# Kernel optimization log

Measured on AMD Instinct MI355X. Metric: run time of the kernel, lower is better.

## Reference

```python
import jax, jax.numpy as jnp
import numpy as np

NUM_HEADS = 16


def setup_inputs() -> dict:
    key = jax.random.key(0)
    ks = jax.random.split(key, 6)
    B, S, D = 2, 2048, 1024
    hidden_states = jax.random.normal(ks[0], (B, S, D), dtype=jnp.float32)
    attention_mask = jnp.zeros((B, 1, 1, S), dtype=jnp.float32)  # additive mask
    # Linear weights stored as [in, out] (equivalent to torch weight.T)
    W_qkv = jax.random.normal(ks[1], (D, 3 * D), dtype=jnp.float32) * (1.0 / np.sqrt(D))
    b_qkv = jnp.zeros((3 * D,), dtype=jnp.float32)
    W_proj = jax.random.normal(ks[2], (D, D), dtype=jnp.float32) * (1.0 / np.sqrt(D))
    b_proj = jnp.zeros((D,), dtype=jnp.float32)
    return {
        "hidden_states": hidden_states,
        "attention_mask": attention_mask,
        "W_qkv": W_qkv,
        "b_qkv": b_qkv,
        "W_proj": W_proj,
        "b_proj": b_proj,
    }


def reference(hidden_states, attention_mask, W_qkv, b_qkv, W_proj, b_proj):
    B, S, D = hidden_states.shape
    H = NUM_HEADS
    hd = D // H
    scale = 1.0 / jnp.sqrt(jnp.asarray(hd, hidden_states.dtype))

    qkv = hidden_states @ W_qkv + b_qkv            # [B,S,3D]
    q, k, v = jnp.split(qkv, 3, axis=-1)
    # [B,S,D] -> [B,H,S,hd]
    split_heads = lambda t: t.reshape(B, S, H, hd).transpose(0, 2, 1, 3)
    q, k, v = split_heads(q), split_heads(k), split_heads(v)

    scores = jnp.einsum("bhqd,bhkd->bhqk", q, k) * scale + attention_mask
    attn = jax.nn.softmax(scores, axis=-1)
    ctx = jnp.einsum("bhqk,bhkd->bhqd", attn, v)   # [B,H,S,hd]
    ctx = ctx.transpose(0, 2, 1, 3).reshape(B, S, D)
    return ctx @ W_proj + b_proj
```

## Files before the change

### kernel.cpp

```cpp
#include <hip/hip_runtime.h>
#include <hip/hip_bf16.h>

typedef short short8 __attribute__((ext_vector_type(8)));
typedef float floatx4 __attribute__((ext_vector_type(4)));
typedef int intx4 __attribute__((ext_vector_type(4)));

#define S_LEN 2048
#define DMODEL 1024
#define NH 16
#define HD 64
#define BATCH 2

static __device__ __forceinline__ short f2bf(float x) {
    __hip_bfloat16 h = __float2bfloat16(x);
    return *(short*)&h;
}

static __device__ __forceinline__ unsigned pk2(float lo, float hi) {
    unsigned a = (unsigned)(unsigned short)f2bf(lo);
    unsigned b = (unsigned)(unsigned short)f2bf(hi);
    return a | (b << 16);
}

static __device__ __forceinline__ void async_ld16(const __hip_bfloat16* g, __hip_bfloat16* l) {
    __builtin_amdgcn_global_load_lds(
        (const __attribute__((address_space(1))) unsigned int*)g,
        (__attribute__((address_space(3))) unsigned int*)l, 16, 0, 0);
}

__global__ __launch_bounds__(256) void cvt_kernel(const float* __restrict__ X,
                                                  __hip_bfloat16* __restrict__ Y) {
    int i = (blockIdx.x * 256 + threadIdx.x) * 8;
    floatx4 f0 = *(const floatx4*)&X[i];
    floatx4 f1 = *(const floatx4*)&X[i + 4];
    short8 s;
    s[0] = f2bf(f0[0]); s[1] = f2bf(f0[1]); s[2] = f2bf(f0[2]); s[3] = f2bf(f0[3]);
    s[4] = f2bf(f1[0]); s[5] = f2bf(f1[1]); s[6] = f2bf(f1[2]); s[7] = f2bf(f1[3]);
    *(short8*)&Y[i] = s;
}

__global__ void transpose_kernel(const float* __restrict__ W,
                                 __hip_bfloat16* __restrict__ Wt, int K, int N) {
    __shared__ float tile[32][33];
    int n0 = blockIdx.x * 32, k0 = blockIdx.y * 32;
    int tx = threadIdx.x, ty = threadIdx.y;
#pragma unroll
    for (int i = 0; i < 32; i += 8)
        tile[ty + i][tx] = W[(size_t)(k0 + ty + i) * N + n0 + tx];
    __syncthreads();
#pragma unroll
    for (int i = 0; i < 32; i += 8)
        Wt[(size_t)(n0 + ty + i) * K + k0 + tx] = __float2bfloat16(tile[tx][ty + i]);
}

__global__ __launch_bounds__(256) void gemm128(
    const __hip_bfloat16* __restrict__ A, const __hip_bfloat16* __restrict__ Bt,
    const float* __restrict__ bias, float* __restrict__ Cf,
    __hip_bfloat16* __restrict__ Qp, __hip_bfloat16* __restrict__ Kp,
    __hip_bfloat16* __restrict__ Vt, int M, int N, int K, int mode) {
    __shared__ __align__(16) __hip_bfloat16 As[128 * 32];
    __shared__ __align__(16) __hip_bfloat16 Bs[128 * 32];
    const int m0 = blockIdx.y * 128, n0 = blockIdx.x * 128;
    const int t = threadIdx.x;
    const int wave = t >> 6, lane = t & 63;
    const int quad = lane >> 4, m16 = lane & 15;
    const int wm = (wave >> 1) * 64, wn = (wave & 1) * 64;
    const int srow = lane >> 2, scol = (lane & 3) * 8;

    floatx4 acc[4][4] = {};
    for (int k0 = 0; k0 < K; k0 += 32) {
#pragma unroll
        for (int i = 0; i < 2; i++) {
            const int rbase = wave * 32 + i * 16;
            async_ld16(&A[(size_t)(m0 + rbase + srow) * K + k0 + scol], &As[rbase * 32]);
            async_ld16(&Bt[(size_t)(n0 + rbase + srow) * K + k0 + scol], &Bs[rbase * 32]);
        }
        __syncthreads();
        short8 af[4], bfr[4];
#pragma unroll
        for (int i = 0; i < 4; i++)
            af[i] = *(const short8*)&As[(wm + i * 16 + m16) * 32 + quad * 8];
#pragma unroll
        for (int j = 0; j < 4; j++)
            bfr[j] = *(const short8*)&Bs[(wn + j * 16 + m16) * 32 + quad * 8];
#pragma unroll
        for (int i = 0; i < 4; i++)
#pragma unroll
            for (int j = 0; j < 4; j++)
                acc[i][j] = __builtin_amdgcn_mfma_f32_16x16x32_bf16(af[i], bfr[j], acc[i][j], 0, 0, 0);
        __syncthreads();
    }
#pragma unroll
    for (int i = 0; i < 4; i++)
#pragma unroll
        for (int j = 0; j < 4; j++) {
            int col = n0 + wn + j * 16 + m16;
            float bv = bias[col];
#pragma unroll
            for (int r = 0; r < 4; r++) {
                int row = m0 + wm + i * 16 + quad * 4 + r;
                float v = acc[i][j][r] + bv;
                if (mode == 0) {
                    Cf[(size_t)row * N + col] = v;
                } else {
                    __hip_bfloat16 hv = __float2bfloat16(v);
                    int tt = col >> 10, rem = col & 1023;
                    int h = rem >> 6, d = rem & 63;
                    int b = row >> 11, s = row & 2047;
                    if (tt == 0)      Qp[((size_t)(b * NH + h) * S_LEN + s) * HD + d] = hv;
                    else if (tt == 1) Kp[((size_t)(b * NH + h) * S_LEN + s) * HD + d] = hv;
                    else              Vt[((size_t)(b * NH + h) * HD + d) * S_LEN + s] = hv;
                }
            }
        }
}

__global__ __launch_bounds__(512, 8) void attn_kernel(
    const __hip_bfloat16* __restrict__ Q,
    const __hip_bfloat16* __restrict__ K,
    const __hip_bfloat16* __restrict__ Vt,
    const float* __restrict__ mask,
    __hip_bfloat16* __restrict__ ctx) {
    __shared__ __align__(16) __hip_bfloat16 smem[16384];
    const int bh = blockIdx.x;
    const int b = bh >> 4, h = bh & 15;
    const int t = threadIdx.x, wave = t >> 6, lane = t & 63;
    const int team = wave >> 2, tw = wave & 3;
    const int quad = lane >> 4, m16 = lane & 15;
    const int qbase = blockIdx.y * 64 + tw * 16;
    const int ko = team * (S_LEN / 2);
    const __hip_bfloat16* Qh = Q + (size_t)bh * S_LEN * HD;
    const __hip_bfloat16* Kh = K + (size_t)bh * S_LEN * HD;
    const __hip_bfloat16* Vh = Vt + (size_t)bh * HD * S_LEN;
    const float* mb = mask + (size_t)b * S_LEN;
    const float LOG2E = 1.44269504f;
    const float scale2 = 0.125f * LOG2E;
    const float M_FIX2 = 20.0f * LOG2E;

    __hip_bfloat16* Ksb = smem + team * 8192;
    __hip_bfloat16* Vsb = smem + team * 8192 + 4096;

    const int kr = lane >> 3, kc = lane & 7;
    const int kgoff = (tw * 8 + kr) * HD + ((kc ^ kr) * 8);
    const int vr = lane >> 2, vc = lane & 3;
    const int vd = tw * 16 + vr;
    const int vgoff = vd * S_LEN + (((vc ^ ((vd >> 1) & 3))) * 8);
    __hip_bfloat16* kdst0 = Ksb + tw * 512;
    __hip_bfloat16* kdst1 = Ksb + 2048 + tw * 512;
    __hip_bfloat16* vdst0 = Vsb + tw * 512;
    __hip_bfloat16* vdst1 = Vsb + 2048 + tw * 512;

    short8 aq0 = *(const short8*)&Qh[(size_t)(qbase + m16) * HD + quad * 8];
    short8 aq1 = *(const short8*)&Qh[(size_t)(qbase + m16) * HD + 32 + quad * 8];

    const short ONEB = (short)0x3F80;
    const short8 ones = {ONEB, ONEB, ONEB, ONEB, ONEB, ONEB, ONEB, ONEB};

    async_ld16(&Kh[(size_t)ko * HD + kgoff], kdst0);
    async_ld16(&Vh[(size_t)ko + vgoff], vdst0);
    __syncthreads();

    floatx4 o[4] = {};
    floatx4 lacc = {};
    const int swk = m16 & 7;
    const int e = quad & 1;
    const int C = ((quad & 1) << 1) | (quad >> 1);
    const int vsl = (C ^ ((m16 >> 1) & 3)) * 8;

    const int NIT = (S_LEN / 2) / 32;
    for (int it = 0; it < NIT; it++) {
        const int k0 = it * 32;
        const int cur = it & 1;
        if (it < NIT - 1) {
            async_ld16(&Kh[(size_t)(ko + k0 + 32) * HD + kgoff], cur ? kdst0 : kdst1);
            async_ld16(&Vh[(size_t)(ko + k0 + 32) + vgoff], cur ? vdst0 : vdst1);
        }

        const __hip_bfloat16* Kc = Ksb + cur * 2048;
        floatx4 sc[2] = {};
        __builtin_amdgcn_s_setprio(1);
#pragma unroll
        for (int kt = 0; kt < 2; kt++) {
            const int row = kt * 16 + m16;
            short8 ak0 = *(const short8*)&Kc[row * 64 + ((quad ^ swk) * 8)];
            short8 ak1 = *(const short8*)&Kc[row * 64 + (((quad + 4) ^ swk) * 8)];
            sc[kt] = __builtin_amdgcn_mfma_f32_16x16x32_bf16(ak0, aq0, sc[kt], 0, 0, 0);
            sc[kt] = __builtin_amdgcn_mfma_f32_16x16x32_bf16(ak1, aq1, sc[kt], 0, 0, 0);
        }
        __builtin_amdgcn_s_setprio(0);

        unsigned dk[2][2];
#pragma unroll
        for (int kt = 0; kt < 2; kt++) {
            floatx4 mv = *(const floatx4*)&mb[ko + k0 + kt * 16 + quad * 4];
            float p0 = __builtin_amdgcn_exp2f(
                __builtin_fmaf(sc[kt][0], scale2, __builtin_fmaf(mv[0], LOG2E, -M_FIX2)));
            float p1 = __builtin_amdgcn_exp2f(
                __builtin_fmaf(sc[kt][1], scale2, __builtin_fmaf(mv[1], LOG2E, -M_FIX2)));
            float p2 = __builtin_amdgcn_exp2f(
                __builtin_fmaf(sc[kt][2], scale2, __builtin_fmaf(mv[2], LOG2E, -M_FIX2)));
            float p3 = __builtin_amdgcn_exp2f(
                __builtin_fmaf(sc[kt][3], scale2, __builtin_fmaf(mv[3], LOG2E, -M_FIX2)));
            dk[kt][0] = pk2(p0, p1);
            dk[kt][1] = pk2(p2, p3);
        }

        unsigned s0 = e ? dk[0][0] : dk[1][0];
        unsigned s1 = e ? dk[0][1] : dk[1][1];
        unsigned r0 = (unsigned)__builtin_amdgcn_ds_swizzle((int)s0, 0x401F);
        unsigned r1 = (unsigned)__builtin_amdgcn_ds_swizzle((int)s1, 0x401F);
        intx4 wa;
        wa[0] = (int)(e ? r0 : dk[0][0]);
        wa[1] = (int)(e ? r1 : dk[0][1]);
        wa[2] = (int)(e ? dk[1][0] : r0);
        wa[3] = (int)(e ? dk[1][1] : r1);
        short8 ap = *(short8*)&wa;

        const __hip_bfloat16* Vc = Vsb + cur * 2048;
        __builtin_amdgcn_s_setprio(1);
        lacc = __builtin_amdgcn_mfma_f32_16x16x32_bf16(ap, ones, lacc, 0, 0, 0);
#pragma unroll
        for (int tt = 0; tt < 4; tt++) {
            const int d = tt * 16 + m16;
            short8 bv = *(const short8*)&Vc[d * 32 + vsl];
            o[tt] = __builtin_amdgcn_mfma_f32_16x16x32_bf16(ap, bv, o[tt], 0, 0, 0);
        }
        __builtin_amdgcn_s_setprio(0);
        __syncthreads();
    }

    float* xch = (float*)smem;
    const int xi = (tw * 64 + lane) * 21;
    if (team == 1) {
#pragma unroll
        for (int tt = 0; tt < 4; tt++)
#pragma unroll
            for (int r = 0; r < 4; r++) xch[xi + tt * 4 + r] = o[tt][r];
#pragma unroll
        for (int r = 0; r < 4; r++) xch[xi + 16 + r] = lacc[r];
    }
    __syncthreads();
    if (team == 0) {
        float li[4];
#pragma unroll
        for (int r = 0; r < 4; r++) li[r] = 1.0f / (lacc[r] + xch[xi + 16 + r]);
#pragma unroll
        for (int tt = 0; tt < 4; tt++)
#pragma unroll
            for (int r = 0; r < 4; r++) {
                int srow = qbase + quad * 4 + r;
                int d = tt * 16 + m16;
                float v = (o[tt][r] + xch[xi + tt * 4 + r]) * li[r];
                ctx[((size_t)b * S_LEN + srow) * DMODEL + h * HD + d] = __float2bfloat16(v);
            }
    }
}

extern "C" void kernel_launch(void* const* d_in, const int* in_sizes, int n_in,
                              void* d_out, int out_size, void* d_ws, size_t ws_size,
                              hipStream_t stream) {
    (void)in_sizes; (void)n_in; (void)out_size; (void)ws_size;
    const float* hidden = (const float*)d_in[0];
    const float* mask   = (const float*)d_in[1];
    const float* Wqkv   = (const float*)d_in[2];
    const float* bqkv   = (const float*)d_in[3];
    const float* Wproj  = (const float*)d_in[4];
    const float* bproj  = (const float*)d_in[5];
    float* out = (float*)d_out;

    __hip_bfloat16* ws = (__hip_bfloat16*)d_ws;
    const size_t Q4 = 4u * 1024 * 1024;
    __hip_bfloat16* Qp      = ws;
    __hip_bfloat16* Kp      = ws + 1 * Q4;
    __hip_bfloat16* Vt      = ws + 2 * Q4;
    __hip_bfloat16* hid_bf  = ws + 3 * Q4;
    __hip_bfloat16* ctx     = ws + 3 * Q4;
    __hip_bfloat16* Wqkv_t  = ws + 4 * Q4;
    __hip_bfloat16* Wproj_t = ws + 4 * Q4;

    cvt_kernel<<<dim3(4 * 1024 * 1024 / 2048), 256, 0, stream>>>(hidden, hid_bf);
    transpose_kernel<<<dim3(3072 / 32, 1024 / 32), dim3(32, 8), 0, stream>>>(Wqkv, Wqkv_t, 1024, 3072);

    gemm128<<<dim3(3072 / 128, 4096 / 128), 256, 0, stream>>>(
        hid_bf, Wqkv_t, bqkv, nullptr, Qp, Kp, Vt, BATCH * S_LEN, 3 * DMODEL, DMODEL, 1);

    transpose_kernel<<<dim3(1024 / 32, 1024 / 32), dim3(32, 8), 0, stream>>>(Wproj, Wproj_t, 1024, 1024);

    attn_kernel<<<dim3(BATCH * NH, S_LEN / 64), 512, 0, stream>>>(Qp, Kp, Vt, mask, ctx);

    gemm128<<<dim3(1024 / 128, 4096 / 128), 256, 0, stream>>>(
        ctx, Wproj_t, bproj, out, nullptr, nullptr, nullptr, BATCH * S_LEN, DMODEL, DMODEL, 0);
}
```

Baseline: 218.7 us.

## Stage V-transpose epilogue through LDS and precompute mask bias in shared memory

The QKV GEMM epilogue for the V third now packs results into LDS with an XOR swizzle. Each wave takes a turn writing, and the block then stores the transposed Vt rows as 16-byte contiguous vectors instead of scattered 2-byte stores. The attention kernel precomputes the scaled additive mask (mask*log2e - fix) once per block into a shared float array. This replaces a per-iteration global load plus FMA with an LDS read. The changes add barriers in the GEMM epilogue and 8 KB more LDS per attention block, which could reduce occupancy.

Measured after the change: 223.7 us. 1.02x slower.

```diff
diff --git a/kernel.cpp b/kernel.cpp
--- a/kernel.cpp
+++ b/kernel.cpp
@@ -4,6 +4,7 @@
 typedef short short8 __attribute__((ext_vector_type(8)));
 typedef float floatx4 __attribute__((ext_vector_type(4)));
 typedef int intx4 __attribute__((ext_vector_type(4)));
+typedef int intx2 __attribute__((ext_vector_type(2)));
 
 #define S_LEN 2048
 #define DMODEL 1024
@@ -90,29 +91,76 @@
                 acc[i][j] = __builtin_amdgcn_mfma_f32_16x16x32_bf16(af[i], bfr[j], acc[i][j], 0, 0, 0);
         __syncthreads();
     }
-#pragma unroll
-    for (int i = 0; i < 4; i++)
-#pragma unroll
-        for (int j = 0; j < 4; j++) {
-            int col = n0 + wn + j * 16 + m16;
-            float bv = bias[col];
-#pragma unroll
-            for (int r = 0; r < 4; r++) {
-                int row = m0 + wm + i * 16 + quad * 4 + r;
-                float v = acc[i][j][r] + bv;
-                if (mode == 0) {
-                    Cf[(size_t)row * N + col] = v;
-                } else {
-                    __hip_bfloat16 hv = __float2bfloat16(v);
+    if (mode == 0) {
+#pragma unroll
+        for (int i = 0; i < 4; i++)
+#pragma unroll
+            for (int j = 0; j < 4; j++) {
+                int col = n0 + wn + j * 16 + m16;
+                float bv = bias[col];
+#pragma unroll
+                for (int r = 0; r < 4; r++) {
+                    int row = m0 + wm + i * 16 + quad * 4 + r;
+                    Cf[(size_t)row * N + col] = acc[i][j][r] + bv;
+                }
+            }
+    } else if (n0 < 2 * DMODEL) {
+#pragma unroll
+        for (int i = 0; i < 4; i++)
+#pragma unroll
+            for (int j = 0; j < 4; j++) {
+                int col = n0 + wn + j * 16 + m16;
+                float bv = bias[col];
+#pragma unroll
+                for (int r = 0; r < 4; r++) {
+                    int row = m0 + wm + i * 16 + quad * 4 + r;
+                    __hip_bfloat16 hv = __float2bfloat16(acc[i][j][r] + bv);
                     int tt = col >> 10, rem = col & 1023;
                     int h = rem >> 6, d = rem & 63;
                     int b = row >> 11, s = row & 2047;
-                    if (tt == 0)      Qp[((size_t)(b * NH + h) * S_LEN + s) * HD + d] = hv;
-                    else if (tt == 1) Kp[((size_t)(b * NH + h) * S_LEN + s) * HD + d] = hv;
-                    else              Vt[((size_t)(b * NH + h) * HD + d) * S_LEN + s] = hv;
+                    if (tt == 0) Qp[((size_t)(b * NH + h) * S_LEN + s) * HD + d] = hv;
+                    else         Kp[((size_t)(b * NH + h) * S_LEN + s) * HD + d] = hv;
                 }
             }
-        }
+    } else {
+        char* T = (char*)As;
+        const int bq = m0 >> 11;
+        const int s_base = m0 & 2047;
+        for (int p = 0; p < 4; p++) {
+            if (wave == p) {
+#pragma unroll
+                for (int j = 0; j < 4; j++) {
+                    const int drow = j * 16 + m16;
+                    const float bv = bias[n0 + wn + j * 16 + m16];
+                    const int within = (quad & 1) * 4;
+#pragma unroll
+                    for (int i = 0; i < 4; i++) {
+                        const int colc = i * 2 + (quad >> 1);
+                        const int physc = colc ^ (drow & 7);
+                        intx2 v;
+                        v[0] = (int)pk2(acc[i][j][0] + bv, acc[i][j][1] + bv);
+                        v[1] = (int)pk2(acc[i][j][2] + bv, acc[i][j][3] + bv);
+                        *(intx2*)(T + drow * 128 + physc * 16 + within * 2) = v;
+                    }
+                }
+            }
+            __syncthreads();
+            {
+                const int dl = t >> 2;
+                const int sseg = (t & 3) * 16;
+                const int c0 = (sseg >> 3) ^ (dl & 7);
+                const int c1 = ((sseg >> 3) + 1) ^ (dl & 7);
+                short8 a0 = *(const short8*)(T + dl * 128 + c0 * 16);
+                short8 a1 = *(const short8*)(T + dl * 128 + c1 * 16);
+                const int hh = (n0 - 2 * DMODEL + (p & 1) * 64) >> 6;
+                const int sg = s_base + (p >> 1) * 64 + sseg;
+                __hip_bfloat16* dst = &Vt[((size_t)(bq * NH + hh) * HD + dl) * S_LEN + sg];
+                *(short8*)dst = a0;
+                *(short8*)(dst + 8) = a1;
+            }
+            __syncthreads();
+        }
+    }
 }
 
 __global__ __launch_bounds__(512, 8) void attn_kernel(
@@ -122,6 +170,7 @@
     const float* __restrict__ mask,
     __hip_bfloat16* __restrict__ ctx) {
     __shared__ __align__(16) __hip_bfloat16 smem[16384];
+    __shared__ float wsm[S_LEN];
     const int bh = blockIdx.x;
     const int b = bh >> 4, h = bh & 15;
     const int t = threadIdx.x, wave = t >> 6, lane = t & 63;
@@ -140,6 +189,14 @@
     __hip_bfloat16* Ksb = smem + team * 8192;
     __hip_bfloat16* Vsb = smem + team * 8192 + 4096;
 
+    {
+        floatx4 mv = *(const floatx4*)&mb[t * 4];
+        floatx4 wv;
+#pragma unroll
+        for (int r = 0; r < 4; r++) wv[r] = __builtin_fmaf(mv[r], LOG2E, -M_FIX2);
+        *(floatx4*)&wsm[t * 4] = wv;
+    }
+
     const int kr = lane >> 3, kc = lane & 7;
     const int kgoff = (tw * 8 + kr) * HD + ((kc ^ kr) * 8);
     const int vr = lane >> 2, vc = lane & 3;
@@ -192,15 +249,11 @@
         unsigned dk[2][2];
 #pragma unroll
         for (int kt = 0; kt < 2; kt++) {
-            floatx4 mv = *(const floatx4*)&mb[ko + k0 + kt * 16 + quad * 4];
-            float p0 = __builtin_amdgcn_exp2f(
-                __builtin_fmaf(sc[kt][0], scale2, __builtin_fmaf(mv[0], LOG2E, -M_FIX2)));
-            float p1 = __builtin_amdgcn_exp2f(
-                __builtin_fmaf(sc[kt][1], scale2, __builtin_fmaf(mv[1], LOG2E, -M_FIX2)));
-            float p2 = __builtin_amdgcn_exp2f(
-                __builtin_fmaf(sc[kt][2], scale2, __builtin_fmaf(mv[2], LOG2E, -M_FIX2)));
-            float p3 = __builtin_amdgcn_exp2f(
-                __builtin_fmaf(sc[kt][3], scale2, __builtin_fmaf(mv[3], LOG2E, -M_FIX2)));
+            floatx4 wv = *(const floatx4*)&wsm[ko + k0 + kt * 16 + quad * 4];
+            float p0 = __builtin_amdgcn_exp2f(__builtin_fmaf(sc[kt][0], scale2, wv[0]));
+            float p1 = __builtin_amdgcn_exp2f(__builtin_fmaf(sc[kt][1], scale2, wv[1]));
+            float p2 = __builtin_amdgcn_exp2f(__builtin_fmaf(sc[kt][2], scale2, wv[2]));
+            float p3 = __builtin_amdgcn_exp2f(__builtin_fmaf(sc[kt][3], scale2, wv[3]));
             dk[kt][0] = pk2(p0, p1);
             dk[kt][1] = pk2(p2, p3);
         }
```
